# Performance work log

Hardware: AMD Instinct MI355X
Metric: run time of the kernel (lower is better)

The kernel has to match this reference:

```python
import jax, jax.numpy as jnp
import numpy as np

N_NODES = 4194304  # 2**22
LEVELS = 10
COARSE = 8192
RANK = 2
NNZ = 8388608


def _interp_linear(u, N):
    """torch F.interpolate(mode='linear', align_corners=False) along axis 1. u: (B,M,R) -> (B,N,R)."""
    M = u.shape[1]
    pos = (jnp.arange(N, dtype=jnp.float32) + 0.5) * (M / N) - 0.5
    pos = jnp.clip(pos, 0.0, M - 1)
    i0 = jnp.floor(pos).astype(jnp.int32)
    i1 = jnp.minimum(i0 + 1, M - 1)
    w = (pos - i0.astype(jnp.float32))[None, :, None]
    return u[:, i0] * (1.0 - w) + u[:, i1] * w


def _apply_hodlr(diag, u_factors, v_factors, x):
    B, N, _ = x.shape
    y = diag * x
    L = u_factors.shape[0]
    for lvl in range(L):
        num_splits = 2 ** (lvl + 1)
        bs = N // num_splits
        if bs == 0:
            continue
        uc, vc = u_factors[lvl], v_factors[lvl]
        u_full = _interp_linear(uc, N) if uc.shape[1] != N else uc
        v_full = _interp_linear(vc, N) if vc.shape[1] != N else vc
        P = num_splits // 2
        valid = P * 2 * bs
        xv = x[:, :valid].reshape(B, P, 2, bs, 1)
        uv = u_full[:, :valid].reshape(B, P, 2, bs, -1)
        vv = v_full[:, :valid].reshape(B, P, 2, bs, -1)
        xL, xR = xv[:, :, 0], xv[:, :, 1]
        uL, uR = uv[:, :, 0], uv[:, :, 1]
        vL, vR = vv[:, :, 0], vv[:, :, 1]
        xRp = jnp.einsum('bpkr,bpko->bpro', vR, xR)  # (B,P,R,1)
        xLp = jnp.einsum('bpkr,bpko->bpro', vL, xL)
        yL = jnp.einsum('bpkr,bpro->bpko', uL, xRp)  # (B,P,bs,1)
        yR = jnp.einsum('bpkr,bpro->bpko', uR, xLp)
        upd = jnp.stack([yL, yR], axis=2).reshape(B, valid, 1)
        if valid < N:
            upd = jnp.pad(upd, ((0, 0), (0, N - valid), (0, 0)))
        y = y + upd
    return y


def setup_inputs() -> dict:
    key = jax.random.key(0)
    ks = jax.random.split(key, 6)
    diag = jax.random.uniform(ks[0], (1, N_NODES, 1), dtype=jnp.float32)
    u_factors = jax.random.normal(ks[1], (LEVELS, 1, COARSE, RANK), dtype=jnp.float32)
    v_factors = jax.random.normal(ks[2], (LEVELS, 1, COARSE, RANK), dtype=jnp.float32)
    A_values = jax.random.normal(ks[3], (NNZ,), dtype=jnp.float32)
    z = jax.random.normal(ks[4], (1, N_NODES, 1), dtype=jnp.float32)
    A_indices = jax.random.randint(ks[5], (2, NNZ), 0, N_NODES, dtype=jnp.int64) if jax.config.jax_enable_x64 else jax.random.randint(ks[5], (2, NNZ), 0, N_NODES, dtype=jnp.int32)
    return {"diag": diag, "u_factors": u_factors, "v_factors": v_factors,
            "A_values": A_values, "z": z, "A_indices": A_indices, "num_nodes": N_NODES}


def reference(diag, u_factors, v_factors, A_values, z, A_indices, num_nodes):
    N = num_nodes
    w = _apply_hodlr(diag, u_factors, v_factors, z)          # (1,N,1)
    w_flat = w.reshape(N)
    rows, cols = A_indices[0], A_indices[1]
    y_flat = jax.ops.segment_sum(A_values * w_flat[cols], rows, num_segments=N)
    y = y_flat.reshape(1, N, 1)
    loss = jnp.mean((y - z) ** 2)
    return loss
```

## Files before the change

### kernel.cpp

```cpp
#include <hip/hip_runtime.h>

#define N_NODES   4194304
#define LEVELS    10
#define COARSE    8192
#define NNZ_E     8388608
#define NCHUNK    16384
#define NBUCK     256
#define BROWS     16384
#define BSH       14
#define HBLOCKS   1024

static __device__ __forceinline__ unsigned short f2bf(float x) {
    unsigned u = __float_as_uint(x);
    return (unsigned short)((u + 0x7FFFu + ((u >> 16) & 1u)) >> 16);
}
static __device__ __forceinline__ float bf2f(unsigned short h) {
    return __uint_as_float((unsigned)h << 16);
}

__global__ __launch_bounds__(256) void kA_moments(const float* __restrict__ z,
                                                  float2* __restrict__ M,
                                                  float* __restrict__ S,
                                                  float* __restrict__ out) {
    if (blockIdx.x == 0) {
        for (int i = threadIdx.x; i < 2046 * 2; i += 256) S[i] = 0.f;
        if (threadIdx.x == 0) out[0] = 0.f;
    }
    int lane = threadIdx.x & 63;
    int wave = threadIdx.x >> 6;
    int chunk = blockIdx.x * 4 + wave;
    int base = chunk * 256 + lane * 4;
    float4 zv = *(const float4*)(z + base);
    float a0 = 0.f, a1 = 0.f;
    const float* zp = (const float*)&zv;
#pragma unroll
    for (int j = 0; j < 4; ++j) {
        float p = ((float)(base + j) + 0.5f) * (1.0f / 512.0f) - 0.5f;
        p = fminf(fmaxf(p, 0.0f), (float)(COARSE - 1));
        float f = p - floorf(p);
        a0 += zp[j] * (1.0f - f);
        a1 += zp[j] * f;
    }
#pragma unroll
    for (int off = 32; off >= 1; off >>= 1) {
        a0 += __shfl_xor(a0, off, 64);
        a1 += __shfl_xor(a1, off, 64);
    }
    if (lane == 0) M[chunk] = make_float2(a0, a1);
}

__global__ __launch_bounds__(1024) void kB_ssum(const float2* __restrict__ M,
                                                const float* __restrict__ V,
                                                float* __restrict__ S) {
    int lvl = blockIdx.x;
    int t = threadIdx.x;
    const float2* Vl = (const float2*)(V + lvl * COARSE * 2);
    float s0 = 0.f, s1 = 0.f;
    int c0 = t * 16;
#pragma unroll
    for (int cc = 0; cc < 16; ++cc) {
        int c = c0 + cc;
        float2 m = M[c];
        int k = (c > 0) ? ((c - 1) >> 1) : 0;
        int kp = min(k + 1, COARSE - 1);
        float2 vk = Vl[k], vkp = Vl[kp];
        s0 += vk.x * m.x + vkp.x * m.y;
        s1 += vk.y * m.x + vkp.y * m.y;
    }
    int gs = 1 << (9 - lvl);
    int gw = min(gs, 64);
    for (int sh = gw >> 1; sh >= 1; sh >>= 1) {
        s0 += __shfl_xor(s0, sh, 64);
        s1 += __shfl_xor(s1, sh, 64);
    }
    if ((t & (gw - 1)) == 0) {
        int b = t >> (9 - lvl);
        int soff = (2 << lvl) - 2;
        unsafeAtomicAdd(&S[(soff + b) * 2 + 0], s0);
        unsafeAtomicAdd(&S[(soff + b) * 2 + 1], s1);
    }
}

__global__ __launch_bounds__(256) void kC_g(const float* __restrict__ S,
                                            const float* __restrict__ U,
                                            float2* __restrict__ G) {
    int c = blockIdx.x * 256 + threadIdx.x;
    int k = (c > 0) ? ((c - 1) >> 1) : 0;
    int kp = min(k + 1, COARSE - 1);
    float g0 = 0.f, g1 = 0.f;
#pragma unroll
    for (int lvl = 0; lvl < LEVELS; ++lvl) {
        int sib = (c >> (13 - lvl)) ^ 1;
        int soff = (2 << lvl) - 2;
        float2 s = ((const float2*)S)[soff + sib];
        const float2* Ul = (const float2*)(U + lvl * COARSE * 2);
        float2 uk = Ul[k], ukp = Ul[kp];
        g0 += uk.x * s.x + uk.y * s.y;
        g1 += ukp.x * s.x + ukp.y * s.y;
    }
    G[c] = make_float2(g0, g1);
}

__global__ __launch_bounds__(256) void kW(const float* __restrict__ diag,
                                          const float* __restrict__ z,
                                          const float2* __restrict__ G,
                                          unsigned short* __restrict__ wb) {
    int tid = blockIdx.x * 256 + threadIdx.x;
    int base = tid * 4;
    float2 g = G[base >> 8];
    float4 d4 = *(const float4*)(diag + base);
    float4 z4 = *(const float4*)(z + base);
    const float* dp = (const float*)&d4;
    const float* zp = (const float*)&z4;
    ushort4 h4;
    unsigned short* hp = (unsigned short*)&h4;
#pragma unroll
    for (int j = 0; j < 4; ++j) {
        float p = ((float)(base + j) + 0.5f) * (1.0f / 512.0f) - 0.5f;
        p = fminf(fmaxf(p, 0.0f), (float)(COARSE - 1));
        float f = p - floorf(p);
        hp[j] = f2bf(dp[j] * zp[j] + (g.x + f * (g.y - g.x)));
    }
    *(ushort4*)(wb + base) = h4;
}

__global__ __launch_bounds__(256) void kHist(const int* __restrict__ rows,
                                             unsigned int* __restrict__ blockOff) {
    __shared__ unsigned int h[NBUCK];
    int blk = blockIdx.x, t = threadIdx.x;
    h[t] = 0u;
    __syncthreads();
    int base = blk * 8192;
#pragma unroll
    for (int it = 0; it < 8; ++it) {
        int e = base + it * 1024 + t * 4;
        int4 r = *(const int4*)(rows + e);
        atomicAdd(&h[r.x >> BSH], 1u);
        atomicAdd(&h[r.y >> BSH], 1u);
        atomicAdd(&h[r.z >> BSH], 1u);
        atomicAdd(&h[r.w >> BSH], 1u);
    }
    __syncthreads();
    blockOff[t * HBLOCKS + blk] = h[t];
}

__global__ __launch_bounds__(256) void kScan1(unsigned int* __restrict__ blockOff,
                                              unsigned int* __restrict__ total) {
    int b = blockIdx.x, t = threadIdx.x;
    unsigned int* p = blockOff + b * HBLOCKS;
    uint4 v = *(uint4*)(p + t * 4);
    unsigned int s = v.x + v.y + v.z + v.w;
    unsigned int incl = s;
#pragma unroll
    for (int off = 1; off < 64; off <<= 1) {
        unsigned int n = __shfl_up(incl, off, 64);
        if ((t & 63) >= off) incl += n;
    }
    __shared__ unsigned int wsum[4], wbase[4];
    if ((t & 63) == 63) wsum[t >> 6] = incl;
    __syncthreads();
    if (t == 0) {
        unsigned int acc = 0;
        for (int i = 0; i < 4; ++i) { wbase[i] = acc; acc += wsum[i]; }
        total[b] = acc;
    }
    __syncthreads();
    unsigned int excl = wbase[t >> 6] + incl - s;
    uint4 e;
    e.x = excl; e.y = excl + v.x; e.z = e.y + v.y; e.w = e.z + v.z;
    *(uint4*)(p + t * 4) = e;
}

__global__ __launch_bounds__(256) void kBinScatter(const int* __restrict__ rows,
                                                   const int* __restrict__ cols,
                                                   const float* __restrict__ vals,
                                                   const unsigned short* __restrict__ wb,
                                                   const unsigned int* __restrict__ blockOff,
                                                   const unsigned int* __restrict__ total,
                                                   uint2* __restrict__ packed) {
    __shared__ unsigned int ctr[NBUCK];
    __shared__ unsigned int wsum[4], wbase[4];
    int blk = blockIdx.x, t = threadIdx.x;
    unsigned int tv = total[t];
    unsigned int incl = tv;
#pragma unroll
    for (int off = 1; off < 64; off <<= 1) {
        unsigned int n = __shfl_up(incl, off, 64);
        if ((t & 63) >= off) incl += n;
    }
    if ((t & 63) == 63) wsum[t >> 6] = incl;
    __syncthreads();
    if (t == 0) {
        unsigned int a = 0;
        for (int i = 0; i < 4; ++i) { wbase[i] = a; a += wsum[i]; }
    }
    __syncthreads();
    ctr[t] = (wbase[t >> 6] + incl - tv) + blockOff[t * HBLOCKS + blk];
    __syncthreads();

    int base = blk * 8192;
#pragma unroll
    for (int half = 0; half < 2; ++half) {
        int4 r[4], c[4];
        float4 v[4];
#pragma unroll
        for (int j = 0; j < 4; ++j) {
            int e = base + (half * 4 + j) * 1024 + t * 4;
            r[j] = *(const int4*)(rows + e);
            c[j] = *(const int4*)(cols + e);
            v[j] = *(const float4*)(vals + e);
        }
        unsigned short wv[16];
#pragma unroll
        for (int j = 0; j < 4; ++j) {
            const int* cp = (const int*)&c[j];
            wv[j * 4 + 0] = wb[cp[0]];
            wv[j * 4 + 1] = wb[cp[1]];
            wv[j * 4 + 2] = wb[cp[2]];
            wv[j * 4 + 3] = wb[cp[3]];
        }
#pragma unroll
        for (int j = 0; j < 4; ++j) {
            const int* rp = (const int*)&r[j];
            const float* vp = (const float*)&v[j];
#pragma unroll
            for (int k = 0; k < 4; ++k) {
                int row = rp[k];
                float p = vp[k] * bf2f(wv[j * 4 + k]);
                unsigned int pos = atomicAdd(&ctr[row >> BSH], 1u);
                packed[pos] = make_uint2((unsigned)(row & (BROWS - 1)), __float_as_uint(p));
            }
        }
    }
}

__global__ __launch_bounds__(1024) void kBucketAccum(const uint2* __restrict__ packed,
                                                     const unsigned int* __restrict__ total,
                                                     const float* __restrict__ z,
                                                     float* __restrict__ out) {
    __shared__ float acc[BROWS];
    __shared__ unsigned int sb, sn;
    __shared__ unsigned int wsum[4], wbase[4];
    __shared__ float red[16];
    int b = blockIdx.x, t = threadIdx.x;

    unsigned int tv = 0, incl = 0;
    if (t < 256) {
        tv = total[t];
        incl = tv;
#pragma unroll
        for (int off = 1; off < 64; off <<= 1) {
            unsigned int n = __shfl_up(incl, off, 64);
            if ((t & 63) >= off) incl += n;
        }
        if ((t & 63) == 63) wsum[t >> 6] = incl;
    }
    __syncthreads();
    if (t == 0) {
        unsigned int a = 0;
        for (int i = 0; i < 4; ++i) { wbase[i] = a; a += wsum[i]; }
    }
    __syncthreads();
    if (t < 256 && t == b) { sb = wbase[t >> 6] + incl - tv; sn = tv; }
    for (int i = t; i < BROWS / 4; i += 1024) ((float4*)acc)[i] = make_float4(0.f, 0.f, 0.f, 0.f);
    __syncthreads();

    unsigned int s0 = sb, n = sn;
    for (unsigned int i = t; i < n; i += 1024) {
        uint2 e = packed[s0 + i];
        atomicAdd(&acc[e.x], __uint_as_float(e.y));
    }
    __syncthreads();

    float part = 0.f;
    int gbase = b * BROWS;
    for (int i = t; i < BROWS; i += 1024) {
        float d = acc[i] - z[gbase + i];
        part += d * d;
    }
#pragma unroll
    for (int off = 32; off >= 1; off >>= 1) part += __shfl_xor(part, off, 64);
    if ((t & 63) == 0) red[t >> 6] = part;
    __syncthreads();
    if (t == 0) {
        float s = 0.f;
        for (int i = 0; i < 16; ++i) s += red[i];
        unsafeAtomicAdd(out, s * (1.0f / (float)N_NODES));
    }
}

extern "C" void kernel_launch(void* const* d_in, const int* in_sizes, int n_in,
                              void* d_out, int out_size, void* d_ws, size_t ws_size,
                              hipStream_t stream) {
    const float* diag  = (const float*)d_in[0];
    const float* U     = (const float*)d_in[1];
    const float* V     = (const float*)d_in[2];
    const float* Avals = (const float*)d_in[3];
    const float* z     = (const float*)d_in[4];
    const int*   Aidx  = (const int*)d_in[5];
    const int* rows = Aidx;
    const int* cols = Aidx + NNZ_E;

    char* ws = (char*)d_ws;
    size_t off = 0;
    unsigned short* wb = (unsigned short*)(ws + off); off += (size_t)N_NODES * 2;
    uint2* packed      = (uint2*)(ws + off);          off += (size_t)NNZ_E * 8;
    unsigned int* blockOff = (unsigned int*)(ws + off); off += (size_t)NBUCK * HBLOCKS * 4;
    unsigned int* total    = (unsigned int*)(ws + off); off += NBUCK * 4;
    float2* M  = (float2*)(ws + off); off += NCHUNK * 8;
    float*  S  = (float*)(ws + off);  off += 2046 * 2 * 4;
    float2* G  = (float2*)(ws + off); off += NCHUNK * 8;

    kA_moments<<<NCHUNK / 4, 256, 0, stream>>>(z, M, S, (float*)d_out);
    kB_ssum<<<LEVELS, 1024, 0, stream>>>(M, V, S);
    kC_g<<<NCHUNK / 256, 256, 0, stream>>>(S, U, G);
    kW<<<N_NODES / 1024, 256, 0, stream>>>(diag, z, G, wb);

    kHist<<<HBLOCKS, 256, 0, stream>>>(rows, blockOff);
    kScan1<<<NBUCK, 256, 0, stream>>>(blockOff, total);
    kBinScatter<<<HBLOCKS, 256, 0, stream>>>(rows, cols, Avals, wb, blockOff, total, packed);
    kBucketAccum<<<NBUCK, 1024, 0, stream>>>(packed, total, z, (float*)d_out);
}
```

Measured before the change: 346.6 us.

## Pack scatter entries into 32 bits, widen histogram grid, add nontemporal loads

Each binned edge entry now takes 32 bits instead of 64: a 14-bit local row plus an 18-bit truncated float. This halves the traffic of the scatter write and the bucket-accumulate read. The histogram and scatter now run on twice as many blocks with half the edges each, and the level-sum kernel is split into 8 slices per level for more parallelism. Streaming inputs use nontemporal loads. The 18-bit value keeps only about 9 mantissa bits, which costs accuracy in the summed products and the loss.

```diff
diff --git a/kernel.cpp b/kernel.cpp
--- a/kernel.cpp
+++ b/kernel.cpp
@@ -8,7 +8,12 @@
 #define NBUCK     256
 #define BROWS     16384
 #define BSH       14
-#define HBLOCKS   1024
+#define HBLOCKS   2048
+#define EPB       4096
+
+typedef int          v4i __attribute__((ext_vector_type(4)));
+typedef float        v4f __attribute__((ext_vector_type(4)));
+typedef unsigned int v4u __attribute__((ext_vector_type(4)));
 
 static __device__ __forceinline__ unsigned short f2bf(float x) {
     unsigned u = __float_as_uint(x);
@@ -16,6 +21,10 @@
 }
 static __device__ __forceinline__ float bf2f(unsigned short h) {
     return __uint_as_float((unsigned)h << 16);
+}
+static __device__ __forceinline__ unsigned pack18(int lrow, float p) {
+    unsigned u = __float_as_uint(p);
+    return ((unsigned)lrow << 18) | (((u + 0x2000u) >> 14) & 0x3FFFFu);
 }
 
 __global__ __launch_bounds__(256) void kA_moments(const float* __restrict__ z,
@@ -52,13 +61,14 @@
 __global__ __launch_bounds__(1024) void kB_ssum(const float2* __restrict__ M,
                                                 const float* __restrict__ V,
                                                 float* __restrict__ S) {
-    int lvl = blockIdx.x;
+    int lvl = blockIdx.x >> 3;
+    int slice = blockIdx.x & 7;
     int t = threadIdx.x;
     const float2* Vl = (const float2*)(V + lvl * COARSE * 2);
     float s0 = 0.f, s1 = 0.f;
-    int c0 = t * 16;
-#pragma unroll
-    for (int cc = 0; cc < 16; ++cc) {
+    int c0 = slice * 2048 + t * 2;
+#pragma unroll
+    for (int cc = 0; cc < 2; ++cc) {
         int c = c0 + cc;
         float2 m = M[c];
         int k = (c > 0) ? ((c - 1) >> 1) : 0;
@@ -67,14 +77,14 @@
         s0 += vk.x * m.x + vkp.x * m.y;
         s1 += vk.y * m.x + vkp.y * m.y;
     }
-    int gs = 1 << (9 - lvl);
-    int gw = min(gs, 64);
+    int tpg_sh = 12 - lvl;
+    int gw = min(1 << tpg_sh, 64);
     for (int sh = gw >> 1; sh >= 1; sh >>= 1) {
         s0 += __shfl_xor(s0, sh, 64);
         s1 += __shfl_xor(s1, sh, 64);
     }
     if ((t & (gw - 1)) == 0) {
-        int b = t >> (9 - lvl);
+        int b = c0 >> (13 - lvl);
         int soff = (2 << lvl) - 2;
         unsafeAtomicAdd(&S[(soff + b) * 2 + 0], s0);
         unsafeAtomicAdd(&S[(soff + b) * 2 + 1], s1);
@@ -108,8 +118,8 @@
     int tid = blockIdx.x * 256 + threadIdx.x;
     int base = tid * 4;
     float2 g = G[base >> 8];
-    float4 d4 = *(const float4*)(diag + base);
-    float4 z4 = *(const float4*)(z + base);
+    v4f d4 = __builtin_nontemporal_load((const v4f*)(diag + base));
+    v4f z4 = __builtin_nontemporal_load((const v4f*)(z + base));
     const float* dp = (const float*)&d4;
     const float* zp = (const float*)&z4;
     ushort4 h4;
@@ -130,11 +140,11 @@
     int blk = blockIdx.x, t = threadIdx.x;
     h[t] = 0u;
     __syncthreads();
-    int base = blk * 8192;
-#pragma unroll
-    for (int it = 0; it < 8; ++it) {
+    int base = blk * EPB;
+#pragma unroll
+    for (int it = 0; it < 4; ++it) {
         int e = base + it * 1024 + t * 4;
-        int4 r = *(const int4*)(rows + e);
+        v4i r = __builtin_nontemporal_load((const v4i*)(rows + e));
         atomicAdd(&h[r.x >> BSH], 1u);
         atomicAdd(&h[r.y >> BSH], 1u);
         atomicAdd(&h[r.z >> BSH], 1u);
@@ -148,8 +158,9 @@
                                               unsigned int* __restrict__ total) {
     int b = blockIdx.x, t = threadIdx.x;
     unsigned int* p = blockOff + b * HBLOCKS;
-    uint4 v = *(uint4*)(p + t * 4);
-    unsigned int s = v.x + v.y + v.z + v.w;
+    v4u a = *(const v4u*)(p + t * 8);
+    v4u c = *(const v4u*)(p + t * 8 + 4);
+    unsigned int s = a.x + a.y + a.z + a.w + c.x + c.y + c.z + c.w;
     unsigned int incl = s;
 #pragma unroll
     for (int off = 1; off < 64; off <<= 1) {
@@ -166,9 +177,11 @@
     }
     __syncthreads();
     unsigned int excl = wbase[t >> 6] + incl - s;
-    uint4 e;
-    e.x = excl; e.y = excl + v.x; e.z = e.y + v.y; e.w = e.z + v.z;
-    *(uint4*)(p + t * 4) = e;
+    v4u e0, e1;
+    e0.x = excl;        e0.y = e0.x + a.x; e0.z = e0.y + a.y; e0.w = e0.z + a.z;
+    e1.x = e0.w + a.w;  e1.y = e1.x + c.x; e1.z = e1.y + c.y; e1.w = e1.z + c.z;
+    *(v4u*)(p + t * 8) = e0;
+    *(v4u*)(p + t * 8 + 4) = e1;
 }
 
 __global__ __launch_bounds__(256) void kBinScatter(const int* __restrict__ rows,
@@ -177,7 +190,7 @@
                                                    const unsigned short* __restrict__ wb,
                                                    const unsigned int* __restrict__ blockOff,
                                                    const unsigned int* __restrict__ total,
-                                                   uint2* __restrict__ packed) {
+                                                   unsigned int* __restrict__ packed) {
     __shared__ unsigned int ctr[NBUCK];
     __shared__ unsigned int wsum[4], wbase[4];
     int blk = blockIdx.x, t = threadIdx.x;
@@ -198,43 +211,40 @@
     ctr[t] = (wbase[t >> 6] + incl - tv) + blockOff[t * HBLOCKS + blk];
     __syncthreads();
 
-    int base = blk * 8192;
-#pragma unroll
-    for (int half = 0; half < 2; ++half) {
-        int4 r[4], c[4];
-        float4 v[4];
-#pragma unroll
-        for (int j = 0; j < 4; ++j) {
-            int e = base + (half * 4 + j) * 1024 + t * 4;
-            r[j] = *(const int4*)(rows + e);
-            c[j] = *(const int4*)(cols + e);
-            v[j] = *(const float4*)(vals + e);
+    int base = blk * EPB;
+    v4i r[4], c[4];
+    v4f v[4];
+#pragma unroll
+    for (int j = 0; j < 4; ++j) {
+        int e = base + j * 1024 + t * 4;
+        r[j] = __builtin_nontemporal_load((const v4i*)(rows + e));
+        c[j] = __builtin_nontemporal_load((const v4i*)(cols + e));
+        v[j] = __builtin_nontemporal_load((const v4f*)(vals + e));
+    }
+    unsigned short wv[16];
+#pragma unroll
+    for (int j = 0; j < 4; ++j) {
+        const int* cp = (const int*)&c[j];
+        wv[j * 4 + 0] = wb[cp[0]];
+        wv[j * 4 + 1] = wb[cp[1]];
+        wv[j * 4 + 2] = wb[cp[2]];
+        wv[j * 4 + 3] = wb[cp[3]];
+    }
+#pragma unroll
+    for (int j = 0; j < 4; ++j) {
+        const int* rp = (const int*)&r[j];
+        const float* vp = (const float*)&v[j];
+#pragma unroll
+        for (int k = 0; k < 4; ++k) {
+            int row = rp[k];
+            float p = vp[k] * bf2f(wv[j * 4 + k]);
+            unsigned int pos = atomicAdd(&ctr[row >> BSH], 1u);
+            packed[pos] = pack18(row & (BROWS - 1), p);
         }
-        unsigned short wv[16];
-#pragma unroll
-        for (int j = 0; j < 4; ++j) {
-            const int* cp = (const int*)&c[j];
-            wv[j * 4 + 0] = wb[cp[0]];
-            wv[j * 4 + 1] = wb[cp[1]];
-            wv[j * 4 + 2] = wb[cp[2]];
-            wv[j * 4 + 3] = wb[cp[3]];
-        }
-#pragma unroll
-        for (int j = 0; j < 4; ++j) {
-            const int* rp = (const int*)&r[j];
-            const float* vp = (const float*)&v[j];
-#pragma unroll
-            for (int k = 0; k < 4; ++k) {
-                int row = rp[k];
-                float p = vp[k] * bf2f(wv[j * 4 + k]);
-                unsigned int pos = atomicAdd(&ctr[row >> BSH], 1u);
-                packed[pos] = make_uint2((unsigned)(row & (BROWS - 1)), __float_as_uint(p));
-            }
-        }
-    }
-}
-
-__global__ __launch_bounds__(1024) void kBucketAccum(const uint2* __restrict__ packed,
+    }
+}
+
+__global__ __launch_bounds__(1024) void kBucketAccum(const unsigned int* __restrict__ packed,
                                                      const unsigned int* __restrict__ total,
                                                      const float* __restrict__ z,
                                                      float* __restrict__ out) {
@@ -267,8 +277,8 @@
 
     unsigned int s0 = sb, n = sn;
     for (unsigned int i = t; i < n; i += 1024) {
-        uint2 e = packed[s0 + i];
-        atomicAdd(&acc[e.x], __uint_as_float(e.y));
+        unsigned int e = __builtin_nontemporal_load(packed + s0 + i);
+        atomicAdd(&acc[e >> 18], __uint_as_float((e & 0x3FFFFu) << 14));
     }
     __syncthreads();
 
@@ -304,7 +314,7 @@
     char* ws = (char*)d_ws;
     size_t off = 0;
     unsigned short* wb = (unsigned short*)(ws + off); off += (size_t)N_NODES * 2;
-    uint2* packed      = (uint2*)(ws + off);          off += (size_t)NNZ_E * 8;
+    unsigned int* packed = (unsigned int*)(ws + off); off += (size_t)NNZ_E * 4;
     unsigned int* blockOff = (unsigned int*)(ws + off); off += (size_t)NBUCK * HBLOCKS * 4;
     unsigned int* total    = (unsigned int*)(ws + off); off += NBUCK * 4;
     float2* M  = (float2*)(ws + off); off += NCHUNK * 8;
@@ -312,7 +322,7 @@
     float2* G  = (float2*)(ws + off); off += NCHUNK * 8;
 
     kA_moments<<<NCHUNK / 4, 256, 0, stream>>>(z, M, S, (float*)d_out);
-    kB_ssum<<<LEVELS, 1024, 0, stream>>>(M, V, S);
+    kB_ssum<<<LEVELS * 8, 1024, 0, stream>>>(M, V, S);
     kC_g<<<NCHUNK / 256, 256, 0, stream>>>(S, U, G);
     kW<<<N_NODES / 1024, 256, 0, stream>>>(diag, z, G, wb);
 
```

After: 341.6 us. No clear change (-1.4%).
